# Performance work log

Hardware: AMD Instinct MI355X
Metric: run time of the kernel (lower is better)

Reference implementation:

```python
import jax, jax.numpy as jnp
import numpy as np

B, N, E = 2, 2048, 2048
H, G, D = 16, 4, 128          # num_heads, num_kv_groups, head_dim = E // H
HID = 4 * E                    # GeGLU hidden width
EPS = 1e-6


def setup_inputs() -> dict:
    key = jax.random.key(0)
    ks = jax.random.split(key, 8)
    g = lambda k, shape: jax.random.normal(k, shape, jnp.float32) * 0.02
    return {
        "x": jax.random.normal(ks[0], (B, N, E), jnp.float32),
        "wq": g(ks[1], (E, H * D)),
        "wk": g(ks[2], (E, G * D)),
        "wv": g(ks[3], (E, G * D)),
        "wo": g(ks[4], (H * D, E)),
        "w1": g(ks[5], (E, 2 * HID)),   # GeGLU in-proj (value | gate)
        "w2": g(ks[6], (HID, E)),       # GeGLU out-proj
        "norm1_w": jnp.ones((E,), jnp.float32),
        "norm2_w": jnp.ones((E,), jnp.float32),
    }


def _rope_cos_sin(n, d, dtype):
    inv_freq = 1.0 / (10000.0 ** (jnp.arange(0, d, 2, dtype=jnp.float32) / d))
    freqs = jnp.arange(n, dtype=jnp.float32)[:, None] * inv_freq[None, :]  # [n, d/2]
    emb = jnp.concatenate([freqs, freqs], axis=-1)                          # [n, d]
    return jnp.cos(emb).astype(dtype), jnp.sin(emb).astype(dtype)


def _rotate_half(t):
    d2 = t.shape[-1] // 2
    return jnp.concatenate([-t[..., d2:], t[..., :d2]], axis=-1)


def _apply_rope(t, cos, sin):
    # t: [b, h, n, d]; cos/sin: [n, d]
    return t * cos + _rotate_half(t) * sin


def _rmsnorm(x, w):
    var = jnp.mean(jnp.square(x), axis=-1, keepdims=True)
    return x * jax.lax.rsqrt(var + EPS) * w


def reference(x, wq, wk, wv, wo, w1, w2, norm1_w, norm2_w):
    b, n, _ = x.shape
    # q = k = v = x reshaped into heads (pre-projection, as in source)
    qkv = x.reshape(b, n, H, D).transpose(0, 2, 1, 3)  # [b, H, n, D]
    cos, sin = _rope_cos_sin(n, D, x.dtype)
    q_r = _apply_rope(qkv, cos, sin)
    k_r = _apply_rope(qkv, cos, sin)
    # flatten back to [b, n, E]
    q_flat = q_r.transpose(0, 2, 1, 3).reshape(b, n, E)
    k_flat = k_r.transpose(0, 2, 1, 3).reshape(b, n, E)
    v_flat = x  # v untouched by RoPE; flatten == x

    # Grouped-query attention with internal projections
    qh = (q_flat @ wq).reshape(b, n, H, D).transpose(0, 2, 1, 3)       # [b, H, n, D]
    kh = (k_flat @ wk).reshape(b, n, G, D)                              # [b, n, G, D]
    vh = (v_flat @ wv).reshape(b, n, G, D)
    kh = jnp.repeat(kh, H // G, axis=2).transpose(0, 2, 1, 3)           # [b, H, n, D]
    vh = jnp.repeat(vh, H // G, axis=2).transpose(0, 2, 1, 3)

    scale = 1.0 / np.sqrt(D)
    scores = jnp.einsum('bhqd,bhkd->bhqk', qh, kh) * scale
    attn = jax.nn.softmax(scores, axis=-1)                               # [b, H, n, n]
    ctx = jnp.einsum('bhqk,bhkd->bhqd', attn, vh)
    attn_out = ctx.transpose(0, 2, 1, 3).reshape(b, n, H * D) @ wo      # [b, n, E]

    x1 = _rmsnorm(x + attn_out, norm1_w)

    # GeGLU FFN
    uv = x1 @ w1
    u, gate = jnp.split(uv, 2, axis=-1)
    fc = (u * jax.nn.gelu(gate)) @ w2

    x2 = _rmsnorm(x1 + fc, norm2_w)
    return (x2, (k_flat, v_flat), attn)
```

## Files before the change

kernel.cpp:

```cpp
#include <hip/hip_runtime.h>
#include <hip/hip_bf16.h>


using f32x4  = __attribute__((ext_vector_type(4))) float;
using bf16x8 = __attribute__((ext_vector_type(8))) short;
using bf16x4 = __attribute__((ext_vector_type(4))) short;
using u16x4  = __attribute__((ext_vector_type(4))) unsigned short;

#define DEV __device__ __forceinline__

#define ASYNC16(lds, g)                                                        \
  __builtin_amdgcn_global_load_lds(                                           \
      (const __attribute__((address_space(1))) void*)(g),                      \
      (__attribute__((address_space(3))) void*)(lds), 16, 0, 0)

DEV unsigned short f2bf(float f) {
  unsigned int u = __float_as_uint(f);
  return (unsigned short)((u + 0x7fffu + ((u >> 16) & 1u)) >> 16);
}
DEV float bf2f(unsigned short h) {
  return __uint_as_float(((unsigned int)h) << 16);
}

DEV float waveRedSum(float v) {
#pragma unroll
  for (int o = 32; o; o >>= 1) v += __shfl_xor(v, o);
  return v;
}

__global__ __launch_bounds__(256) void kconvT(const float* __restrict__ in,
                                              unsigned short* __restrict__ out,
                                              int K, int N) {
  __shared__ float tile[32][33];
  int bx = blockIdx.x * 32;
  int by = blockIdx.y * 32;
  int tx = threadIdx.x & 31;
  int ty = threadIdx.x >> 5;
#pragma unroll
  for (int i = 0; i < 32; i += 8)
    tile[ty + i][tx] = in[(size_t)(by + ty + i) * N + bx + tx];
  __syncthreads();
#pragma unroll
  for (int i = 0; i < 32; i += 8)
    out[(size_t)(bx + ty + i) * K + by + tx] = f2bf(tile[tx][ty + i]);
}

__global__ __launch_bounds__(256) void kcopy(const f32x4* __restrict__ x,
                                             f32x4* __restrict__ v,
                                             u16x4* __restrict__ xb) {
  int i = blockIdx.x * 256 + threadIdx.x;
  f32x4 val = x[i];
  v[i] = val;
  u16x4 o;
  o[0] = f2bf(val[0]); o[1] = f2bf(val[1]); o[2] = f2bf(val[2]); o[3] = f2bf(val[3]);
  xb[i] = o;
}

__global__ __launch_bounds__(256) void krope(const float* __restrict__ x,
                                             float* __restrict__ kout,
                                             unsigned short* __restrict__ xq) {
  int idx = blockIdx.x * 256 + threadIdx.x;
  int f  = idx & 63;
  int h  = (idx >> 6) & 15;
  int bn = idx >> 10;
  int n  = bn & 2047;
  size_t base = (size_t)bn * 2048 + h * 128;
  float inv = exp2f((float)f * (-13.287712379549449f / 64.0f));
  float ang = (float)n * inv;
  float c = cosf(ang), s = sinf(ang);
  float a = x[base + f], b = x[base + f + 64];
  float k1 = a * c - b * s;
  float k2 = b * c + a * s;
  kout[base + f]      = k1;
  kout[base + f + 64] = k2;
  xq[base + f]      = f2bf(k1);
  xq[base + f + 64] = f2bf(k2);
}

__global__ __launch_bounds__(256) void krms1(const float* __restrict__ x,
                                             const float* __restrict__ ao,
                                             const float* __restrict__ w,
                                             unsigned short* __restrict__ x1b) {
  size_t row = blockIdx.x;
  const f32x4* xp = (const f32x4*)(x + row * 2048);
  const f32x4* ap = (const f32x4*)(ao + row * 2048);
  int tid = threadIdx.x;
  f32x4 t0 = xp[tid * 2] + ap[tid * 2];
  f32x4 t1 = xp[tid * 2 + 1] + ap[tid * 2 + 1];
  float ss = 0.f;
#pragma unroll
  for (int i = 0; i < 4; ++i) ss += t0[i] * t0[i] + t1[i] * t1[i];
  ss = waveRedSum(ss);
  __shared__ float red[4];
  int wid = tid >> 6, lane = tid & 63;
  if (!lane) red[wid] = ss;
  __syncthreads();
  ss = red[0] + red[1] + red[2] + red[3];
  float rr = rsqrtf(ss * (1.0f / 2048.0f) + 1e-6f);
  const f32x4* wp = (const f32x4*)w;
  f32x4 w0 = wp[tid * 2], w1 = wp[tid * 2 + 1];
  u16x4 o0, o1;
#pragma unroll
  for (int i = 0; i < 4; ++i) {
    o0[i] = f2bf(t0[i] * rr * w0[i]);
    o1[i] = f2bf(t1[i] * rr * w1[i]);
  }
  u16x4* op = (u16x4*)(x1b + row * 2048);
  op[tid * 2] = o0;
  op[tid * 2 + 1] = o1;
}

__global__ __launch_bounds__(256) void krms2(const unsigned short* __restrict__ x1b,
                                             const unsigned short* __restrict__ fc,
                                             const float* __restrict__ w,
                                             float* __restrict__ out) {
  size_t row = blockIdx.x;
  const u16x4* xp = (const u16x4*)(x1b + row * 2048);
  const u16x4* fp = (const u16x4*)(fc + row * 2048);
  int tid = threadIdx.x;
  u16x4 a0 = xp[tid * 2], a1 = xp[tid * 2 + 1];
  u16x4 b0 = fp[tid * 2], b1 = fp[tid * 2 + 1];
  f32x4 t0, t1;
#pragma unroll
  for (int i = 0; i < 4; ++i) {
    t0[i] = bf2f(a0[i]) + bf2f(b0[i]);
    t1[i] = bf2f(a1[i]) + bf2f(b1[i]);
  }
  float ss = 0.f;
#pragma unroll
  for (int i = 0; i < 4; ++i) ss += t0[i] * t0[i] + t1[i] * t1[i];
  ss = waveRedSum(ss);
  __shared__ float red[4];
  int wid = tid >> 6, lane = tid & 63;
  if (!lane) red[wid] = ss;
  __syncthreads();
  ss = red[0] + red[1] + red[2] + red[3];
  float rr = rsqrtf(ss * (1.0f / 2048.0f) + 1e-6f);
  const f32x4* wp = (const f32x4*)w;
  f32x4 w0 = wp[tid * 2], w1 = wp[tid * 2 + 1];
  f32x4* op = (f32x4*)(out + row * 2048);
  op[tid * 2]     = t0 * rr * w0;
  op[tid * 2 + 1] = t1 * rr * w1;
}

template <bool OUT_BF16, bool TRANS_OUT>
__global__ __launch_bounds__(256, 2) void gemm_bt(
    const unsigned short* __restrict__ A, const unsigned short* __restrict__ Bt,
    void* __restrict__ C_, int K, int lda, int ldb, int ldc, float alpha) {
  __shared__ unsigned short As[128 * 32];
  __shared__ unsigned short Bs[128 * 32];
  const int tid = threadIdx.x;
  const int bm0 = blockIdx.y * 128, bn0 = blockIdx.x * 128;

  f32x4 acc[4][4] = {};

  const int lane = tid & 63, wid = tid >> 6;
  const int wr = wid >> 1, wc = wid & 1;
  const int lr = lane & 15, kq = lane >> 4;
  const int srow = tid >> 2;
  const int scol = (tid & 3) * 8;
  unsigned short* AsW = As + tid * 8;
  unsigned short* BsW = Bs + tid * 8;

  for (int kt = 0; kt < K; kt += 32) {
    ASYNC16(AsW,        A + (size_t)(bm0 + srow)      * lda + kt + scol);
    ASYNC16(AsW + 2048, A + (size_t)(bm0 + srow + 64) * lda + kt + scol);
    ASYNC16(BsW,        Bt + (size_t)(bn0 + srow)      * ldb + kt + scol);
    ASYNC16(BsW + 2048, Bt + (size_t)(bn0 + srow + 64) * ldb + kt + scol);
    __syncthreads();
    bf16x8 afr[4], bfr[4];
#pragma unroll
    for (int i = 0; i < 4; ++i)
      afr[i] = *(const bf16x8*)&As[(wr * 64 + i * 16 + lr) * 32 + kq * 8];
#pragma unroll
    for (int j = 0; j < 4; ++j)
      bfr[j] = *(const bf16x8*)&Bs[(wc * 64 + j * 16 + lr) * 32 + kq * 8];
#pragma unroll
    for (int i = 0; i < 4; ++i)
#pragma unroll
      for (int j = 0; j < 4; ++j)
        acc[i][j] = __builtin_amdgcn_mfma_f32_16x16x32_bf16(afr[i], bfr[j],
                                                            acc[i][j], 0, 0, 0);
    __syncthreads();
  }

#pragma unroll
  for (int i = 0; i < 4; ++i)
#pragma unroll
    for (int j = 0; j < 4; ++j) {
      int rowb = bm0 + wr * 64 + i * 16 + kq * 4;
      int col = bn0 + wc * 64 + j * 16 + lr;
#pragma unroll
      for (int r = 0; r < 4; ++r) {
        float v = acc[i][j][r] * alpha;
        size_t idx = TRANS_OUT ? ((size_t)col * ldc + (rowb + r))
                               : ((size_t)(rowb + r) * ldc + col);
        if constexpr (OUT_BF16)
          ((unsigned short*)C_)[idx] = f2bf(v);
        else
          ((float*)C_)[idx] = v;
      }
    }
}

__global__ __launch_bounds__(512, 4) void kattn(
    const unsigned short* __restrict__ qh,
    const unsigned short* __restrict__ kh,
    const unsigned short* __restrict__ vT,
    float* __restrict__ attn,
    unsigned short* __restrict__ ctx) {
  __shared__ __align__(16) char U[65536];
  __shared__ __align__(16) char Vb[16384];
  float* redm = (float*)Vb;
  float* reds = redm + 128;

  const int tid = threadIdx.x;
  const int lane = tid & 63, w = tid >> 6;
  const int lr = lane & 15, kq = lane >> 4;
  const int bid = blockIdx.x;
  const int g8 = bid & 7;
  const int j  = bid >> 3;
  const int bz = g8 >> 2;
  const int gz = g8 & 3;
  const int hz = gz * 4 + (j & 3);
  const int q0 = (j >> 2) << 4;
  const int z  = bz * 16 + hz;

  const unsigned short* Aq =
      qh + ((size_t)(bz * 2048 + q0 + lr) * 2048 + hz * 128);
  bf16x8 qfr[4];
#pragma unroll
  for (int kk = 0; kk < 4; ++kk)
    qfr[kk] = *(const bf16x8*)(Aq + kk * 32 + kq * 8);

  const unsigned short* Kb =
      kh + ((size_t)(bz * 2048) * 512 + gz * 128);
  int krow[4], kcs[4];
#pragma unroll
  for (int R = 0; R < 4; ++R) {
    int idx = R * 64 + lane;
    krow[R] = idx >> 4;
    kcs[R] = (idx & 15) ^ (krow[R] & 7);
  }
  auto stageK = [&](int buf, int t) {
#pragma unroll
    for (int R = 0; R < 4; ++R)
      ASYNC16(U + buf * 32768 + w * 4096 + (R * 64 + lane) * 16,
              Kb + (size_t)(t * 128 + w * 16 + krow[R]) * 512 + kcs[R] * 8);
  };

  f32x4 acc[16];
#pragma unroll
  for (int t = 0; t < 16; ++t) acc[t] = f32x4{0.f, 0.f, 0.f, 0.f};

  stageK(0, 0);
  stageK(1, 1);
#pragma unroll
  for (int t = 0; t < 16; ++t) {
    if (t < 15) asm volatile("s_waitcnt vmcnt(4)" ::: "memory");
    else        asm volatile("s_waitcnt vmcnt(0)" ::: "memory");
    __builtin_amdgcn_sched_barrier(0);
    const char* Kw = U + (t & 1) * 32768 + w * 4096;
    bf16x8 kfr[4];
#pragma unroll
    for (int kk = 0; kk < 4; ++kk) {
      int cch = (kk * 4 + kq) ^ (lr & 7);
      kfr[kk] = *(const bf16x8*)(Kw + lr * 256 + cch * 16);
    }
    asm volatile("s_waitcnt lgkmcnt(0)" ::: "memory");
    __builtin_amdgcn_sched_barrier(0);
    if (t + 2 < 16) stageK(t & 1, t + 2);
#pragma unroll
    for (int kk = 0; kk < 4; ++kk)
      acc[t] = __builtin_amdgcn_mfma_f32_16x16x32_bf16(kfr[kk], qfr[kk],
                                                       acc[t], 0, 0, 0);
  }

  const float scale = 0.08838834764831845f;
  float mx = -3.4e38f;
#pragma unroll
  for (int t = 0; t < 16; ++t) {
    acc[t] *= scale;
#pragma unroll
    for (int r = 0; r < 4; ++r) mx = fmaxf(mx, acc[t][r]);
  }
  mx = fmaxf(mx, __shfl_xor(mx, 16));
  mx = fmaxf(mx, __shfl_xor(mx, 32));
  if (kq == 0) redm[w * 16 + lr] = mx;
  __syncthreads();
  mx = redm[lr];
#pragma unroll
  for (int ww = 1; ww < 8; ++ww) mx = fmaxf(mx, redm[ww * 16 + lr]);

  float sm = 0.f;
#pragma unroll
  for (int t = 0; t < 16; ++t) {
#pragma unroll
    for (int r = 0; r < 4; ++r) {
      float e = __expf(acc[t][r] - mx);
      acc[t][r] = e;
      sm += e;
    }
  }
  sm += __shfl_xor(sm, 16);
  sm += __shfl_xor(sm, 32);
  if (kq == 0) reds[w * 16 + lr] = sm;
  __syncthreads();
  float smt = reds[lr];
#pragma unroll
  for (int ww = 1; ww < 8; ++ww) smt += reds[ww * 16 + lr];
  float inv = 1.0f / smt;

  float* arow = attn + (((size_t)z * 2048 + q0 + lr) * 2048);
#pragma unroll
  for (int t = 0; t < 16; ++t) {
    int key = t * 128 + w * 16 + kq * 4;
    f32x4 p = acc[t] * inv;
    *(f32x4*)(arow + key) = p;
    bf16x4 pb;
#pragma unroll
    for (int r = 0; r < 4; ++r) pb[r] = (short)f2bf(p[r]);
    int c8 = key >> 3;
    *(bf16x4*)(U + lr * 4096 + ((c8 ^ (lr & 7)) << 4) + ((key & 7) << 1)) = pb;
  }
  __syncthreads();

  const unsigned short* Bv = vT + (size_t)gz * 524288 + bz * 2048;
  const int d0 = w * 16;
  const int vd = lane >> 2;
  const int vcs = (lane & 3) ^ (vd & 3);
  auto stageV = [&](int buf, int t) {
    ASYNC16(Vb + buf * 8192 + w * 1024 + lane * 16,
            Bv + (size_t)(d0 + vd) * 4096 + t * 32 + vcs * 8);
  };

  f32x4 cfr = {};
  stageV(0, 0);
  stageV(1, 1);
#pragma unroll
  for (int t = 0; t < 64; ++t) {
    if (t < 63) asm volatile("s_waitcnt vmcnt(1)" ::: "memory");
    else        asm volatile("s_waitcnt vmcnt(0)" ::: "memory");
    __builtin_amdgcn_sched_barrier(0);
    int c8 = t * 4 + kq;
    bf16x8 pfr = *(const bf16x8*)(U + lr * 4096 + ((c8 ^ (lr & 7)) << 4));
    const char* Vw = Vb + (t & 1) * 8192 + w * 1024;
    bf16x8 vfr = *(const bf16x8*)(Vw + lr * 64 + ((kq ^ (lr & 3)) << 4));
    asm volatile("s_waitcnt lgkmcnt(0)" ::: "memory");
    __builtin_amdgcn_sched_barrier(0);
    if (t + 2 < 64) stageV(t & 1, t + 2);
    cfr = __builtin_amdgcn_mfma_f32_16x16x32_bf16(pfr, vfr, cfr, 0, 0, 0);
  }
#pragma unroll
  for (int r = 0; r < 4; ++r) {
    int q = kq * 4 + r;
    ctx[((size_t)(bz * 2048 + q0 + q) * 2048) + hz * 128 + d0 + lr] =
        f2bf(cfr[r]);
  }
}

template <bool OUT_BF16>
__global__ __launch_bounds__(512, 2) void gemm256(
    const unsigned short* __restrict__ A, const unsigned short* __restrict__ Bt,
    void* __restrict__ C_, int K, int lda, int ldb, int ldc) {
  __shared__ unsigned short As[2][256 * 64];
  __shared__ unsigned short Bs[2][128 * 64];
  const int tid = threadIdx.x;
  const int bm0 = blockIdx.y * 256, bn0 = blockIdx.x * 128;
  const int lane = tid & 63, wid = tid >> 6;
  const int wr = wid >> 2, wc = wid & 3;
  const int lr = lane & 15, kq = lane >> 4;

  f32x4 acc[8][2] = {};

  int sArow[4], sAcc[4], sBrow[2], sBcc[2];
#pragma unroll
  for (int R = 0; R < 4; ++R) {
    int c = R * 512 + tid;
    sArow[R] = c >> 3;
    sAcc[R]  = (c & 7) ^ (sArow[R] & 7);
  }
#pragma unroll
  for (int R = 0; R < 2; ++R) {
    int c = R * 512 + tid;
    sBrow[R] = c >> 3;
    sBcc[R]  = (c & 7) ^ (sBrow[R] & 7);
  }

  auto stage = [&](int buf, int k0) {
#pragma unroll
    for (int R = 0; R < 4; ++R)
      ASYNC16(&As[buf][(R * 512 + tid) * 8],
              A + (size_t)(bm0 + sArow[R]) * lda + k0 + sAcc[R] * 8);
#pragma unroll
    for (int R = 0; R < 2; ++R)
      ASYNC16(&Bs[buf][(R * 512 + tid) * 8],
              Bt + (size_t)(bn0 + sBrow[R]) * ldb + k0 + sBcc[R] * 8);
  };

  const int NT = K >> 6;
  stage(0, 0);
  __syncthreads();
  int cur = 0;
  for (int t = 0; t < NT; ++t) {
    if (t + 1 < NT) stage(cur ^ 1, (t + 1) << 6);
    const unsigned short* Ac = As[cur];
    const unsigned short* Bc = Bs[cur];
    __builtin_amdgcn_s_setprio(1);
#pragma unroll
    for (int ks = 0; ks < 2; ++ks) {
      bf16x8 afr[8];
#pragma unroll
      for (int i = 0; i < 8; ++i) {
        int row = wr * 128 + i * 16 + lr;
        int cch = (ks * 4 + kq) ^ (row & 7);
        afr[i] = *(const bf16x8*)&Ac[(row * 8 + cch) * 8];
      }
#pragma unroll
      for (int j = 0; j < 2; ++j) {
        int brow = wc * 32 + j * 16 + lr;
        int cch = (ks * 4 + kq) ^ (brow & 7);
        bf16x8 bfr = *(const bf16x8*)&Bc[(brow * 8 + cch) * 8];
#pragma unroll
        for (int i = 0; i < 8; ++i)
          acc[i][j] = __builtin_amdgcn_mfma_f32_16x16x32_bf16(afr[i], bfr,
                                                              acc[i][j], 0, 0, 0);
      }
    }
    __builtin_amdgcn_s_setprio(0);
    __syncthreads();
    cur ^= 1;
  }

#pragma unroll
  for (int i = 0; i < 8; ++i)
#pragma unroll
    for (int j = 0; j < 2; ++j) {
      int rowb = bm0 + wr * 128 + i * 16 + kq * 4;
      int col = bn0 + wc * 32 + j * 16 + lr;
#pragma unroll
      for (int r = 0; r < 4; ++r) {
        if constexpr (OUT_BF16)
          ((unsigned short*)C_)[(size_t)(rowb + r) * ldc + col] = f2bf(acc[i][j][r]);
        else
          ((float*)C_)[(size_t)(rowb + r) * ldc + col] = acc[i][j][r];
      }
    }
}

__global__ __launch_bounds__(512, 2) void gemm_geglu256(
    const unsigned short* __restrict__ A, const unsigned short* __restrict__ B1,
    const unsigned short* __restrict__ B2, unsigned short* __restrict__ H_,
    int K, int lda, int ldb, int ldc) {
  __shared__ unsigned short As[2][256 * 64];
  __shared__ unsigned short B1s[2][128 * 64];
  __shared__ unsigned short B2s[2][128 * 64];
  const int tid = threadIdx.x;
  const int bm0 = blockIdx.y * 256, bn0 = blockIdx.x * 128;
  const int lane = tid & 63, wid = tid >> 6;
  const int wr = wid >> 2, wc = wid & 3;
  const int lr = lane & 15, kq = lane >> 4;

  f32x4 accu[8][2] = {};
  f32x4 accg[8][2] = {};

  int sArow[4], sAcc[4], sBrow[2], sBcc[2];
#pragma unroll
  for (int R = 0; R < 4; ++R) {
    int c = R * 512 + tid;
    sArow[R] = c >> 3;
    sAcc[R]  = (c & 7) ^ (sArow[R] & 7);
  }
#pragma unroll
  for (int R = 0; R < 2; ++R) {
    int c = R * 512 + tid;
    sBrow[R] = c >> 3;
    sBcc[R]  = (c & 7) ^ (sBrow[R] & 7);
  }

  auto stage = [&](int buf, int k0) {
#pragma unroll
    for (int R = 0; R < 4; ++R)
      ASYNC16(&As[buf][(R * 512 + tid) * 8],
              A + (size_t)(bm0 + sArow[R]) * lda + k0 + sAcc[R] * 8);
#pragma unroll
    for (int R = 0; R < 2; ++R)
      ASYNC16(&B1s[buf][(R * 512 + tid) * 8],
              B1 + (size_t)(bn0 + sBrow[R]) * ldb + k0 + sBcc[R] * 8);
#pragma unroll
    for (int R = 0; R < 2; ++R)
      ASYNC16(&B2s[buf][(R * 512 + tid) * 8],
              B2 + (size_t)(bn0 + sBrow[R]) * ldb + k0 + sBcc[R] * 8);
  };

  const int NT = K >> 6;
  stage(0, 0);
  __syncthreads();
  int cur = 0;
  for (int t = 0; t < NT; ++t) {
    if (t + 1 < NT) stage(cur ^ 1, (t + 1) << 6);
    const unsigned short* Ac = As[cur];
    const unsigned short* B1c = B1s[cur];
    const unsigned short* B2c = B2s[cur];
    __builtin_amdgcn_s_setprio(1);
#pragma unroll
    for (int ks = 0; ks < 2; ++ks) {
      bf16x8 afr[8];
#pragma unroll
      for (int i = 0; i < 8; ++i) {
        int row = wr * 128 + i * 16 + lr;
        int cch = (ks * 4 + kq) ^ (row & 7);
        afr[i] = *(const bf16x8*)&Ac[(row * 8 + cch) * 8];
      }
#pragma unroll
      for (int j = 0; j < 2; ++j) {
        int brow = wc * 32 + j * 16 + lr;
        int cch = (ks * 4 + kq) ^ (brow & 7);
        bf16x8 b1 = *(const bf16x8*)&B1c[(brow * 8 + cch) * 8];
        bf16x8 b2 = *(const bf16x8*)&B2c[(brow * 8 + cch) * 8];
#pragma unroll
        for (int i = 0; i < 8; ++i) {
          accu[i][j] = __builtin_amdgcn_mfma_f32_16x16x32_bf16(afr[i], b1,
                                                               accu[i][j], 0, 0, 0);
          accg[i][j] = __builtin_amdgcn_mfma_f32_16x16x32_bf16(afr[i], b2,
                                                               accg[i][j], 0, 0, 0);
        }
      }
    }
    __builtin_amdgcn_s_setprio(0);
    __syncthreads();
    cur ^= 1;
  }

#pragma unroll
  for (int i = 0; i < 8; ++i)
#pragma unroll
    for (int j = 0; j < 2; ++j) {
      int rowb = bm0 + wr * 128 + i * 16 + kq * 4;
      int col = bn0 + wc * 32 + j * 16 + lr;
#pragma unroll
      for (int r = 0; r < 4; ++r) {
        float u = accu[i][j][r];
        float g = accg[i][j][r];
        float tv = tanhf(0.7978845608028654f * (g + 0.044715f * g * g * g));
        float hv = u * 0.5f * g * (1.0f + tv);
        H_[(size_t)(rowb + r) * ldc + col] = f2bf(hv);
      }
    }
}

extern "C" void kernel_launch(void* const* d_in, const int* in_sizes, int n_in,
                              void* d_out, int out_size, void* d_ws, size_t ws_size,
                              hipStream_t stream) {
  const float* x   = (const float*)d_in[0];
  const float* wq  = (const float*)d_in[1];
  const float* wk  = (const float*)d_in[2];
  const float* wv  = (const float*)d_in[3];
  const float* wo  = (const float*)d_in[4];
  const float* w1  = (const float*)d_in[5];
  const float* w2  = (const float*)d_in[6];
  const float* n1w = (const float*)d_in[7];
  const float* n2w = (const float*)d_in[8];

  float* out    = (float*)d_out;
  float* x2_out = out;
  float* k_out  = out + 8388608;
  float* v_out  = out + 16777216;
  float* attn   = out + 25165824;

  char* ws = (char*)d_ws;
  unsigned short* wqT  = (unsigned short*)(ws + 0);
  unsigned short* wkT  = (unsigned short*)(ws + 8388608);
  unsigned short* wvT  = (unsigned short*)(ws + 10485760);
  unsigned short* woT  = (unsigned short*)(ws + 12582912);
  unsigned short* w1T  = (unsigned short*)(ws + 20971520);
  unsigned short* w2T  = (unsigned short*)(ws + 88080384);
  unsigned short* qh   = (unsigned short*)(ws + 121634816);
  unsigned short* kh   = (unsigned short*)(ws + 138412032);
  unsigned short* vhT  = (unsigned short*)(ws + 142606336);
  unsigned short* ctx  = (unsigned short*)(ws + 146800640);
  float*          ao   = (float*)(ws + 163577856);
  unsigned short* hbuf = (unsigned short*)(ws + 121634816);
  unsigned short* x1b  = (unsigned short*)(ws + 197132288);
  unsigned short* fc   = (unsigned short*)(ws + 213909504);

  unsigned short* xb = (unsigned short*)attn;
  unsigned short* xq = xb + 8388608;

  dim3 blk(256);
  dim3 blk512(512);

  kconvT<<<dim3(64, 64), blk, 0, stream>>>(wq, wqT, 2048, 2048);
  kconvT<<<dim3(16, 64), blk, 0, stream>>>(wk, wkT, 2048, 512);
  kconvT<<<dim3(16, 64), blk, 0, stream>>>(wv, wvT, 2048, 512);
  kconvT<<<dim3(64, 64), blk, 0, stream>>>(wo, woT, 2048, 2048);
  kconvT<<<dim3(512, 64), blk, 0, stream>>>(w1, w1T, 2048, 16384);
  kconvT<<<dim3(64, 256), blk, 0, stream>>>(w2, w2T, 8192, 2048);

  kcopy<<<8192, blk, 0, stream>>>((const f32x4*)x, (f32x4*)v_out, (u16x4*)xb);
  krope<<<16384, blk, 0, stream>>>(x, k_out, xq);

  gemm256<true><<<dim3(16, 16), blk512, 0, stream>>>(
      xq, wqT, qh, 2048, 2048, 2048, 2048);
  gemm_bt<true, false><<<dim3(4, 32), blk, 0, stream>>>(
      xq, wkT, kh, 2048, 2048, 2048, 512, 1.0f);
  gemm_bt<true, true><<<dim3(4, 32), blk, 0, stream>>>(
      xb, wvT, vhT, 2048, 2048, 2048, 4096, 1.0f);

  kattn<<<dim3(4096), blk512, 0, stream>>>(qh, kh, vhT, attn, ctx);

  gemm256<false><<<dim3(16, 16), blk512, 0, stream>>>(
      ctx, woT, (void*)ao, 2048, 2048, 2048, 2048);
  krms1<<<4096, blk, 0, stream>>>(x, ao, n1w, x1b);
  gemm_geglu256<<<dim3(64, 16), blk512, 0, stream>>>(
      x1b, w1T, w1T + 16777216, hbuf, 2048, 2048, 2048, 8192);
  gemm256<true><<<dim3(16, 16), blk512, 0, stream>>>(
      hbuf, w2T, fc, 8192, 8192, 8192, 2048);
  krms2<<<4096, blk, 0, stream>>>(x1b, fc, n2w, x2_out);
}
```

Baseline: 1.114 ms.

## Deepen GEMM K-loop prefetch to two tiles with explicit vmcnt waits and split barriers

Restructures the double-buffered K loop of the plain GEMM and the fused GeGLU GEMM. Two tiles are prefetched up front, and each iteration waits with a partial vmcnt rather than a full syncthreads. The second half-tile's fragments are read into registers before a mid-iteration barrier, after which the freed buffer is refilled for tile t+2. This gives the global-to-LDS copies a full iteration of MFMA work to hide behind. The cost is more registers, and the hand-set waitcnt values must match the number of async loads issued per stage.

```diff
diff --git a/kernel.cpp b/kernel.cpp
--- a/kernel.cpp
+++ b/kernel.cpp
@@ -400,35 +400,59 @@
 
   const int NT = K >> 6;
   stage(0, 0);
-  __syncthreads();
+  stage(1, 64);
   int cur = 0;
   for (int t = 0; t < NT; ++t) {
-    if (t + 1 < NT) stage(cur ^ 1, (t + 1) << 6);
+    if (t + 1 < NT) asm volatile("s_waitcnt vmcnt(6)" ::: "memory");
+    else            asm volatile("s_waitcnt vmcnt(0)" ::: "memory");
+    __builtin_amdgcn_sched_barrier(0);
+    __builtin_amdgcn_s_barrier();
+    __builtin_amdgcn_sched_barrier(0);
     const unsigned short* Ac = As[cur];
     const unsigned short* Bc = Bs[cur];
+    bf16x8 afr0[8], bfr0[2];
+#pragma unroll
+    for (int i = 0; i < 8; ++i) {
+      int row = wr * 128 + i * 16 + lr;
+      afr0[i] = *(const bf16x8*)&Ac[(row * 8 + (kq ^ (row & 7))) * 8];
+    }
+#pragma unroll
+    for (int j2 = 0; j2 < 2; ++j2) {
+      int brow = wc * 32 + j2 * 16 + lr;
+      bfr0[j2] = *(const bf16x8*)&Bc[(brow * 8 + (kq ^ (brow & 7))) * 8];
+    }
     __builtin_amdgcn_s_setprio(1);
 #pragma unroll
-    for (int ks = 0; ks < 2; ++ks) {
-      bf16x8 afr[8];
-#pragma unroll
-      for (int i = 0; i < 8; ++i) {
-        int row = wr * 128 + i * 16 + lr;
-        int cch = (ks * 4 + kq) ^ (row & 7);
-        afr[i] = *(const bf16x8*)&Ac[(row * 8 + cch) * 8];
-      }
-#pragma unroll
-      for (int j = 0; j < 2; ++j) {
-        int brow = wc * 32 + j * 16 + lr;
-        int cch = (ks * 4 + kq) ^ (brow & 7);
-        bf16x8 bfr = *(const bf16x8*)&Bc[(brow * 8 + cch) * 8];
-#pragma unroll
-        for (int i = 0; i < 8; ++i)
-          acc[i][j] = __builtin_amdgcn_mfma_f32_16x16x32_bf16(afr[i], bfr,
-                                                              acc[i][j], 0, 0, 0);
-      }
-    }
+    for (int j2 = 0; j2 < 2; ++j2)
+#pragma unroll
+      for (int i = 0; i < 8; ++i)
+        acc[i][j2] = __builtin_amdgcn_mfma_f32_16x16x32_bf16(afr0[i], bfr0[j2],
+                                                             acc[i][j2], 0, 0, 0);
     __builtin_amdgcn_s_setprio(0);
-    __syncthreads();
+    bf16x8 afr1[8], bfr1[2];
+#pragma unroll
+    for (int i = 0; i < 8; ++i) {
+      int row = wr * 128 + i * 16 + lr;
+      afr1[i] = *(const bf16x8*)&Ac[(row * 8 + ((4 + kq) ^ (row & 7))) * 8];
+    }
+#pragma unroll
+    for (int j2 = 0; j2 < 2; ++j2) {
+      int brow = wc * 32 + j2 * 16 + lr;
+      bfr1[j2] = *(const bf16x8*)&Bc[(brow * 8 + ((4 + kq) ^ (brow & 7))) * 8];
+    }
+    asm volatile("s_waitcnt lgkmcnt(0)" ::: "memory");
+    __builtin_amdgcn_sched_barrier(0);
+    __builtin_amdgcn_s_barrier();
+    __builtin_amdgcn_sched_barrier(0);
+    if (t + 2 < NT) stage(cur, (t + 2) << 6);
+    __builtin_amdgcn_s_setprio(1);
+#pragma unroll
+    for (int j2 = 0; j2 < 2; ++j2)
+#pragma unroll
+      for (int i = 0; i < 8; ++i)
+        acc[i][j2] = __builtin_amdgcn_mfma_f32_16x16x32_bf16(afr1[i], bfr1[j2],
+                                                             acc[i][j2], 0, 0, 0);
+    __builtin_amdgcn_s_setprio(0);
     cur ^= 1;
   }
 
@@ -495,40 +519,68 @@
 
   const int NT = K >> 6;
   stage(0, 0);
-  __syncthreads();
+  stage(1, 64);
   int cur = 0;
   for (int t = 0; t < NT; ++t) {
-    if (t + 1 < NT) stage(cur ^ 1, (t + 1) << 6);
+    if (t + 1 < NT) asm volatile("s_waitcnt vmcnt(8)" ::: "memory");
+    else            asm volatile("s_waitcnt vmcnt(0)" ::: "memory");
+    __builtin_amdgcn_sched_barrier(0);
+    __builtin_amdgcn_s_barrier();
+    __builtin_amdgcn_sched_barrier(0);
     const unsigned short* Ac = As[cur];
     const unsigned short* B1c = B1s[cur];
     const unsigned short* B2c = B2s[cur];
+    bf16x8 afr0[8], b10[2], b20[2];
+#pragma unroll
+    for (int i = 0; i < 8; ++i) {
+      int row = wr * 128 + i * 16 + lr;
+      afr0[i] = *(const bf16x8*)&Ac[(row * 8 + (kq ^ (row & 7))) * 8];
+    }
+#pragma unroll
+    for (int j2 = 0; j2 < 2; ++j2) {
+      int brow = wc * 32 + j2 * 16 + lr;
+      b10[j2] = *(const bf16x8*)&B1c[(brow * 8 + (kq ^ (brow & 7))) * 8];
+      b20[j2] = *(const bf16x8*)&B2c[(brow * 8 + (kq ^ (brow & 7))) * 8];
+    }
     __builtin_amdgcn_s_setprio(1);
 #pragma unroll
-    for (int ks = 0; ks < 2; ++ks) {
-      bf16x8 afr[8];
+    for (int j2 = 0; j2 < 2; ++j2)
 #pragma unroll
       for (int i = 0; i < 8; ++i) {
-        int row = wr * 128 + i * 16 + lr;
-        int cch = (ks * 4 + kq) ^ (row & 7);
-        afr[i] = *(const bf16x8*)&Ac[(row * 8 + cch) * 8];
+        accu[i][j2] = __builtin_amdgcn_mfma_f32_16x16x32_bf16(afr0[i], b10[j2],
+                                                              accu[i][j2], 0, 0, 0);
+        accg[i][j2] = __builtin_amdgcn_mfma_f32_16x16x32_bf16(afr0[i], b20[j2],
+                                                              accg[i][j2], 0, 0, 0);
       }
-#pragma unroll
-      for (int j = 0; j < 2; ++j) {
-        int brow = wc * 32 + j * 16 + lr;
-        int cch = (ks * 4 + kq) ^ (brow & 7);
-        bf16x8 b1 = *(const bf16x8*)&B1c[(brow * 8 + cch) * 8];
-        bf16x8 b2 = *(const bf16x8*)&B2c[(brow * 8 + cch) * 8];
-#pragma unroll
-        for (int i = 0; i < 8; ++i) {
-          accu[i][j] = __builtin_amdgcn_mfma_f32_16x16x32_bf16(afr[i], b1,
-                                                               accu[i][j], 0, 0, 0);
-          accg[i][j] = __builtin_amdgcn_mfma_f32_16x16x32_bf16(afr[i], b2,
-                                                               accg[i][j], 0, 0, 0);
-        }
+    __builtin_amdgcn_s_setprio(0);
+    bf16x8 afr1[8], b11[2], b21[2];
+#pragma unroll
+    for (int i = 0; i < 8; ++i) {
+      int row = wr * 128 + i * 16 + lr;
+      afr1[i] = *(const bf16x8*)&Ac[(row * 8 + ((4 + kq) ^ (row & 7))) * 8];
+    }
+#pragma unroll
+    for (int j2 = 0; j2 < 2; ++j2) {
+      int brow = wc * 32 + j2 * 16 + lr;
+      b11[j2] = *(const bf16x8*)&B1c[(brow * 8 + ((4 + kq) ^ (brow & 7))) * 8];
+      b21[j2] = *(const bf16x8*)&B2c[(brow * 8 + ((4 + kq) ^ (brow & 7))) * 8];
+    }
+    asm volatile("s_waitcnt lgkmcnt(0)" ::: "memory");
+    __builtin_amdgcn_sched_barrier(0);
+    __builtin_amdgcn_s_barrier();
+    __builtin_amdgcn_sched_barrier(0);
+    if (t + 2 < NT) stage(cur, (t + 2) << 6);
+    __builtin_amdgcn_s_setprio(1);
+#pragma unroll
+    for (int j2 = 0; j2 < 2; ++j2)
+#pragma unroll
+      for (int i = 0; i < 8; ++i) {
+        accu[i][j2] = __builtin_amdgcn_mfma_f32_16x16x32_bf16(afr1[i], b11[j2],
+                                                              accu[i][j2], 0, 0, 0);
+        accg[i][j2] = __builtin_amdgcn_mfma_f32_16x16x32_bf16(afr1[i], b21[j2],
+                                                              accg[i][j2], 0, 0, 0);
       }
-    }
     __builtin_amdgcn_s_setprio(0);
-    __syncthreads();
     cur ^= 1;
   }
 
```

New measurement: 1.059 ms. -4.9%, faster.
